# Performance work log

Measured on AMD Instinct MI355X. Metric: run time of the kernel, lower is better.

Reference implementation:

```python
import jax, jax.numpy as jnp
import numpy as np

NUM_CLASSES = 2
TOP_K = 5000
NMS_THRESH = 0.3
CONF_THRESH = 0.05
VAR0, VAR1 = 0.1, 0.2


def setup_inputs() -> dict:
    key = jax.random.key(0)
    k1, k2, k3 = jax.random.split(key, 3)
    B, P = 4, 32768
    loc_data = jax.random.normal(k1, (B, P, 4), dtype=jnp.float32)
    conf_data = jax.random.uniform(k2, (B, P, NUM_CLASSES), dtype=jnp.float32)
    prior_data = jax.random.uniform(k3, (P, 4), dtype=jnp.float32)
    return {"loc_data": loc_data, "conf_data": conf_data, "prior_data": prior_data}


def _detect(loc_data, conf_data, prior_data):
    B = loc_data.shape[0]
    P = prior_data.shape[0]
    loc = loc_data.reshape(B, P, 4)
    conf = conf_data.reshape(B, P, NUM_CLASSES)

    # decode: priors are (cx, cy, w, h); output corner boxes (x1, y1, x2, y2)
    cxcy = prior_data[None, :, :2] + loc[..., :2] * VAR0 * prior_data[None, :, 2:]
    wh = prior_data[None, :, 2:] * jnp.exp(loc[..., 2:] * VAR1)
    boxes = jnp.concatenate([cxcy - 0.5 * wh, cxcy + 0.5 * wh], axis=-1)  # [B,P,4]

    def per_image(bx, sc):  # bx: [P,4], sc: [P] (class-1 scores)
        valid = sc > CONF_THRESH
        masked = jnp.where(valid, sc, -jnp.inf)
        order = jnp.argsort(-masked)[:TOP_K]        # top_k candidates, score-descending
        cb = bx[order]                              # [K,4]
        cs = sc[order]                              # [K]
        cv = valid[order]                           # [K]

        x1, y1, x2, y2 = cb[:, 0], cb[:, 1], cb[:, 2], cb[:, 3]
        area = (x2 - x1) * (y2 - y1)                # [K]
        # pairwise IoU matrix [K,K]
        iw = jnp.maximum(jnp.minimum(x2[:, None], x2[None, :]) - jnp.maximum(x1[:, None], x1[None, :]), 0.0)
        ih = jnp.maximum(jnp.minimum(y2[:, None], y2[None, :]) - jnp.maximum(y1[:, None], y1[None, :]), 0.0)
        inter = iw * ih
        union = area[:, None] + area[None, :] - inter
        suppress = (inter / union) > NMS_THRESH     # suppress if IoU > thresh (keep if <=)

        def step(suppressed, j):
            keep_j = cv[j] & jnp.logical_not(suppressed[j])
            suppressed = suppressed | (keep_j & suppress[j])
            return suppressed, keep_j

        _, kept = jax.lax.scan(step, jnp.zeros((TOP_K,), bool), jnp.arange(TOP_K))

        # pack kept detections (score, x1, y1, x2, y2) to the front, zeros elsewhere
        pos = jnp.where(kept, jnp.cumsum(kept.astype(jnp.int32)) - 1, TOP_K)
        rows = jnp.concatenate([cs[:, None], cb], axis=1)  # [K,5]
        return jnp.zeros((TOP_K, 5), loc_data.dtype).at[pos].set(rows, mode='drop')

    out1 = jax.vmap(per_image)(boxes, conf[..., 1])  # [B,K,5]
    output = jnp.zeros((B, NUM_CLASSES, TOP_K, 5), loc_data.dtype)
    return output.at[:, 1].set(out1)  # class 0 (background) stays zero


def reference(loc_data, conf_data, prior_data):
    return _detect(loc_data, conf_data, prior_data)
```

## Files before the change

### kernel.cpp

```cpp
#include <hip/hip_runtime.h>
#include <hip/hip_bf16.h>
#include <math.h>

#define BB 4
#define PP 32768
#define TOPK 5000
#define NB 4096
#define NBK 20
#define TBPI 210
#define BMW 160
#define TRIW 411872u

#define NV_OFF     0u
#define NC_OFF     64u
#define CS_OFF     256u
#define CB_OFF     80256u
#define HIST_OFF   400256u
#define CNT_OFF    465792u
#define START_OFF  531328u
#define GIDX_OFF   596864u
#define GSC_OFF    1121152u
#define BM_OFF     400256u
#define WS_NEEDED  3742720u

typedef const __attribute__((address_space(1))) unsigned GU1;
struct U4p { unsigned x, y, z, w; };
typedef const __attribute__((address_space(1))) U4p GU4;

__device__ __forceinline__ unsigned toffw(unsigned r) {
    unsigned q = r >> 5, s = r & 31u;
    return r * 160u - 16u * q * (q - 1u) - s * q;
}

__global__ __launch_bounds__(256) void score_hist_kernel(
    const float2* __restrict__ conf, unsigned* __restrict__ hist,
    float2* __restrict__ outz, int outn2)
{
    int i = blockIdx.x * 256 + threadIdx.x;
    if (i < outn2) outz[i] = make_float2(0.0f, 0.0f);
    if (i >= BB * PP) return;
    int b = i >> 15;
    float s = conf[i].y;
    if (s > 0.05f) {
        int bk = (int)(s * 4096.0f);
        bk = bk < 0 ? 0 : (bk > NB - 1 ? NB - 1 : bk);
        atomicAdd(&hist[b * NB + bk], 1u);
    }
}

__global__ __launch_bounds__(256) void scan_hist_kernel(
    const unsigned* __restrict__ hist, unsigned* __restrict__ start,
    int* __restrict__ nvalid, int* __restrict__ ncand)
{
    int b = blockIdx.x;
    int t = threadIdx.x;
    __shared__ unsigned sums[256];
    unsigned local[16];
    unsigned s = 0;
    const unsigned* hb = hist + b * NB;
    #pragma unroll
    for (int k = 0; k < 16; k++) {
        unsigned v = hb[t * 16 + k];
        local[k] = s;
        s += v;
    }
    sums[t] = s;
    __syncthreads();
    for (int off = 1; off < 256; off <<= 1) {
        unsigned v = (t >= off) ? sums[t - off] : 0u;
        __syncthreads();
        sums[t] += v;
        __syncthreads();
    }
    unsigned excl = sums[t] - s;
    unsigned* sb = start + b * NB;
    #pragma unroll
    for (int k = 0; k < 16; k++) sb[t * 16 + k] = excl + local[k];
    if (t == 255) {
        nvalid[b] = (int)sums[255];
        ncand[b] = sums[255] < (unsigned)TOPK ? (int)sums[255] : TOPK;
    }
}

__global__ __launch_bounds__(256) void scatter_group_kernel(
    const float2* __restrict__ conf, const unsigned* __restrict__ start,
    unsigned* __restrict__ cnt, unsigned* __restrict__ gidx,
    float* __restrict__ gscore)
{
    int i = blockIdx.x * 256 + threadIdx.x;
    if (i >= BB * PP) return;
    int b = i >> 15;
    int p = i & (PP - 1);
    float s = conf[i].y;
    if (s > 0.05f) {
        int bk = (int)(s * 4096.0f);
        bk = bk < 0 ? 0 : (bk > NB - 1 ? NB - 1 : bk);
        unsigned o = atomicAdd(&cnt[b * NB + bk], 1u);
        unsigned pos = start[b * NB + bk] + o;
        gidx[b * PP + pos] = (unsigned)p;
        gscore[b * PP + pos] = s;
    }
}

__global__ __launch_bounds__(256) void rank_topk_kernel(
    const unsigned* __restrict__ gidx, const float* __restrict__ gscore,
    const unsigned* __restrict__ start, const unsigned* __restrict__ hist,
    const int* __restrict__ nvalid, const float4* __restrict__ loc,
    const float4* __restrict__ prior,
    float* __restrict__ cs, float4* __restrict__ cb)
{
#pragma clang fp contract(off)
    int i = blockIdx.x * 256 + threadIdx.x;
    if (i >= BB * PP) return;
    int b = i >> 15;
    int pos = i & (PP - 1);
    int nv = nvalid[b];
    if (pos >= nv) return;
    float s = gscore[b * PP + pos];
    unsigned p = gidx[b * PP + pos];
    int bk = (int)(s * 4096.0f);
    bk = bk < 0 ? 0 : (bk > NB - 1 ? NB - 1 : bk);
    unsigned st = start[b * NB + bk];
    unsigned c = hist[b * NB + bk];
    unsigned rank = (unsigned)nv - st - c;
    const float* gs = gscore + b * PP + st;
    const unsigned* gi = gidx + b * PP + st;
    for (unsigned k = 0; k < c; k++) {
        float sk = gs[k];
        unsigned pk = gi[k];
        if (sk > s || (sk == s && pk < p)) rank++;
    }
    if (rank < (unsigned)TOPK) {
        float4 l = loc[b * PP + (int)p];
        float4 pr = prior[p];
        float cx = pr.x + (l.x * 0.1f) * pr.z;
        float cy = pr.y + (l.y * 0.1f) * pr.w;
        float w = pr.z * expf(l.z * 0.2f);
        float h = pr.w * expf(l.w * 0.2f);
        float4 bx;
        bx.x = cx - 0.5f * w;
        bx.y = cy - 0.5f * h;
        bx.z = cx + 0.5f * w;
        bx.w = cy + 0.5f * h;
        cs[b * TOPK + rank] = s;
        cb[(size_t)b * TOPK + rank] = bx;
    }
}

__global__ __launch_bounds__(256) void bitmap_pair_kernel(
    const float4* __restrict__ cb, int img_base, unsigned* __restrict__ bitmap)
{
#pragma clang fp contract(off)
    int p = blockIdx.x / TBPI;
    int t_ = blockIdx.x % TBPI;
    int img = img_base + p;
    unsigned* bmp = bitmap + (size_t)p * TRIW;

    int bi = (int)((sqrtf(8.0f * (float)t_ + 1.0f) - 1.0f) * 0.5f);
    while ((bi + 1) * (bi + 2) / 2 <= t_) bi++;
    while (bi * (bi + 1) / 2 > t_) bi--;
    int bj = t_ - bi * (bi + 1) / 2;

    const float4* cbb = cb + (size_t)img * TOPK;

    __shared__ float4 jb[256];
    __shared__ float ja[256];
    int tid = threadIdx.x;
    int cg = bi * 256 + tid;
    if (cg < TOPK) {
        float4 v = cbb[cg];
        jb[tid] = v;
        ja[tid] = (v.z - v.x) * (v.w - v.y);
    }
    __syncthreads();

    int r = bj * 256 + tid;
    if (r >= TOPK) return;
    float4 bx = cbb[r];
    float areaR = (bx.z - bx.x) * (bx.w - bx.y);
    bool diag = (bi == bj);

    unsigned wds[8];
    #pragma unroll
    for (int w8 = 0; w8 < 8; w8++) {
        unsigned m = 0u;
        int cb0 = w8 * 32;
        for (int k = 0; k < 32; k++) {
            int cl = cb0 + k;
            int c = bi * 256 + cl;
            if (c >= TOPK) break;
            if (diag && c <= r) continue;
            float4 cc = jb[cl];
            float iw = fminf(bx.z, cc.z) - fmaxf(bx.x, cc.x);
            iw = fmaxf(iw, 0.0f);
            float ih = fminf(bx.w, cc.w) - fmaxf(bx.y, cc.y);
            ih = fmaxf(ih, 0.0f);
            float inter = iw * ih;
            float uni = (ja[cl] + areaR) - inter;
            if (inter / uni > 0.3f) m |= (1u << k);
        }
        wds[w8] = m;
    }
    unsigned q = (unsigned)r >> 5;
    unsigned basew = toffw((unsigned)r) - q + 8u * (unsigned)bi;
    int c0 = diag ? (int)(q - 8u * (unsigned)bj) : 0;
    for (int c = c0; c < 8; c++) bmp[basew + (unsigned)c] = wds[c];
}

__global__ __launch_bounds__(576, 1) void solve_scalar_kernel(
    const float* __restrict__ cs, const float4* __restrict__ cb,
    const int* __restrict__ ncand, int img_base,
    const unsigned* __restrict__ bitmap, float* __restrict__ out)
{
    int tid = threadIdx.x;
    int wv = tid >> 6;
    int lane = tid & 63;
    int img = img_base + blockIdx.x;
    int nc = ncand[img];
    const unsigned* bm = bitmap + (size_t)blockIdx.x * TRIW;

    __shared__ __align__(16) unsigned Rl8[8][BMW];
    __shared__ __align__(16) unsigned diab[2][64][4];
    __shared__ unsigned kw[BMW];
    __shared__ unsigned pref[BMW];

    for (int w = tid; w < BMW; w += 576) {
        kw[w] = 0u;
        int lo = w * 32;
        unsigned m;
        if (lo >= nc) m = 0xffffffffu;
        else if (lo + 32 <= nc) m = 0u;
        else m = ~((1u << (nc - lo)) - 1u);
        Rl8[0][w] = m;
    }
    for (int i = tid; i < 7 * BMW; i += 576) Rl8[1 + i / BMW][i % BMW] = 0u;

    int ng = (nc + 63) >> 6;
    unsigned l4 = (unsigned)lane << 2;
    uint4 P0[8], P1[8], P2[8];
    unsigned carry_lo = 0u, carry_hi = 0u;

#define LOADG(BUF, G) do {                                                  \
    int g_ = (G);                                                           \
    if (g_ < ng && lane < 40) {                                             \
        _Pragma("unroll")                                                   \
        for (int rr = 0; rr < 8; rr++) {                                    \
            int j_ = g_ * 64 + (wv - 1) + 8 * rr;                           \
            unsigned jc_ = (unsigned)(j_ < nc ? j_ : nc - 1);               \
            unsigned q_ = jc_ >> 5;                                         \
            GU4* p4_ = (GU4*)(bm + (toffw(jc_) - q_ + l4));                 \
            BUF[rr].x = p4_->x; BUF[rr].y = p4_->y;                         \
            BUF[rr].z = p4_->z; BUF[rr].w = p4_->w;                         \
        }                                                                   \
    }                                                                       \
} while (0)

#define STAGE(SB, G) do {                                                   \
    int g_ = (G);                                                           \
    if (g_ < ng) {                                                          \
        int pa_ = g_ & 1;                                                   \
        if ((g_ & 1) == 0) {                                                \
            int kl_ = g_ >> 1;             \
            if (lane == kl_) {                                              \
                _Pragma("unroll")                                           \
                for (int rr = 0; rr < 8; rr++)                              \
                    *(uint4*)&diab[pa_][(wv - 1) + 8 * rr][0] = SB[rr];     \
            }                                                               \
        } else {                                                            \
            int kl_ = (g_ - 1) >> 1;          \
            if (lane == kl_) {                                              \
                _Pragma("unroll")                                           \
                for (int rr = 0; rr < 8; rr++) {                            \
                    int r_ = (wv - 1) + 8 * rr;                             \
                    diab[pa_][r_][0] = SB[rr].z;                            \
                    diab[pa_][r_][1] = SB[rr].w;                            \
                }                                                           \
            }                                                               \
            if (lane == kl_ + 1) {                                          \
                _Pragma("unroll")                                           \
                for (int rr = 0; rr < 8; rr++) {                            \
                    int r_ = (wv - 1) + 8 * rr;                             \
                    diab[pa_][r_][2] = SB[rr].x;                            \
                    diab[pa_][r_][3] = SB[rr].y;                            \
                }                                                           \
            }                                                               \
        }                                                                   \
    }                                                                       \
} while (0)

#define PHASE(W, FB, SB) do {                                               \
    int w_ = (W);                                                           \
    if (wv == 0) {                                                          \
        int par_ = w_ & 1;                                                  \
        uint2 d01_ = *(const uint2*)&diab[par_][lane][0];                   \
        uint2 d23_ = *(const uint2*)&diab[par_][lane][2];                   \
        unsigned gv_ = 0u;                                                  \
        if (lane < 16) gv_ = Rl8[lane & 7][2 * w_ + (lane >> 3)];           \
        gv_ |= __shfl_xor(gv_, 1);                                          \
        gv_ |= __shfl_xor(gv_, 2);                                          \
        gv_ |= __shfl_xor(gv_, 4);                                          \
        unsigned glo_ = (unsigned)__builtin_amdgcn_readlane((int)gv_, 0);   \
        unsigned ghi_ = (unsigned)__builtin_amdgcn_readlane((int)gv_, 8);   \
        unsigned long long A_ =                                             \
            ~((((unsigned long long)(ghi_ | carry_hi)) << 32)               \
              | (unsigned long long)(glo_ | carry_lo));                     \
        unsigned rlo_ = d01_.x, rhi_ = d01_.y;                              \
        if (lane < 32) rlo_ |= 1u << lane;                                  \
        else           rhi_ |= 1u << (lane & 31);                           \
        unsigned long long K_ = 0ull;                                       \
        while (A_) {                                                        \
            int j_ = __builtin_ctzll(A_);                                   \
            unsigned slo_ = (unsigned)__builtin_amdgcn_readlane((int)rlo_, j_); \
            unsigned shi_ = (unsigned)__builtin_amdgcn_readlane((int)rhi_, j_); \
            K_ |= 1ull << j_;                                               \
            A_ &= ~((((unsigned long long)shi_) << 32)                      \
                    | (unsigned long long)slo_);                            \
        }                                                                   \
        if (lane == 0) {                                                    \
            kw[2 * w_] = (unsigned)K_;                                      \
            kw[2 * w_ + 1] = (unsigned)(K_ >> 32);                          \
        }                                                                   \
        unsigned keep_ = (unsigned)((K_ >> lane) & 1ull);                   \
        unsigned nm_ = 0u - keep_;                                          \
        unsigned nlo_ = d23_.x & nm_, nhi_ = d23_.y & nm_;                  \
        _Pragma("unroll")                                                   \
        for (int mm_ = 32; mm_; mm_ >>= 1) {                                \
            nlo_ |= __shfl_xor(nlo_, mm_);                                  \
            nhi_ |= __shfl_xor(nhi_, mm_);                                  \
        }                                                                   \
        carry_lo = nlo_; carry_hi = nhi_;                                   \
    } else {                                                                \
        if (w_ > 0) {                                                       \
            unsigned klo_ = kw[2 * (w_ - 1)];                               \
            unsigned khi_ = kw[2 * (w_ - 1) + 1];                           \
            unsigned long long Kp_ =                                        \
                (((unsigned long long)khi_) << 32) | klo_;                  \
            uint4 acc_; acc_.x = acc_.y = acc_.z = acc_.w = 0u;             \
            _Pragma("unroll")                                               \
            for (int rr = 0; rr < 8; rr++) {                                \
                int r_ = (wv - 1) + 8 * rr;                                 \
                unsigned a_ = (unsigned)((Kp_ >> r_) & 1ull);               \
                unsigned m_ = 0u - a_;                                      \
                acc_.x |= FB[rr].x & m_; acc_.y |= FB[rr].y & m_;           \
                acc_.z |= FB[rr].z & m_; acc_.w |= FB[rr].w & m_;           \
            }                                                               \
            if (lane < 40) {                                                \
                uint4 cur_ = *(const uint4*)&Rl8[wv - 1][l4];               \
                cur_.x |= acc_.x; cur_.y |= acc_.y;                         \
                cur_.z |= acc_.z; cur_.w |= acc_.w;                         \
                *(uint4*)&Rl8[wv - 1][l4] = cur_;                           \
            }                                                               \
        }                                                                   \
        STAGE(SB, w_ + 1);                                                  \
        LOADG(FB, w_ + 2);                                                  \
    }                                                                       \
    asm volatile("s_waitcnt lgkmcnt(0)" ::: "memory");                      \
    __builtin_amdgcn_s_barrier();                                           \
} while (0)

    if (wv > 0) {
        LOADG(P0, 0);
        LOADG(P1, 1);
    }
    __syncthreads();
    if (wv > 0) STAGE(P0, 0);
    __syncthreads();

    for (int w = 0; w < ng; ) {
        PHASE(w, P2, P1); ++w; if (w >= ng) break;
        PHASE(w, P0, P2); ++w; if (w >= ng) break;
        PHASE(w, P1, P0); ++w;
    }
#undef LOADG
#undef STAGE
#undef PHASE

    __syncthreads();
    if (tid == 0) {
        unsigned s = 0;
        for (int w = 0; w < BMW; w++) { pref[w] = s; s += __popc(kw[w]); }
    }
    __syncthreads();

    const float* csb = cs + img * TOPK;
    const float4* cbb = cb + (size_t)img * TOPK;
    float* outb = out + ((size_t)img * 2 + 1) * TOPK * 5;
    for (int i = tid; i < nc; i += 576) {
        unsigned w = kw[i >> 5];
        if ((w >> (i & 31)) & 1u) {
            unsigned pos = pref[i >> 5] + __popc(w & ((1u << (i & 31)) - 1u));
            float4 bx = cbb[i];
            float* row = outb + (size_t)pos * 5;
            row[0] = csb[i];
            row[1] = bx.x;
            row[2] = bx.y;
            row[3] = bx.z;
            row[4] = bx.w;
        }
    }
}

extern "C" void kernel_launch(void* const* d_in, const int* in_sizes, int n_in,
                              void* d_out, int out_size, void* d_ws, size_t ws_size,
                              hipStream_t stream) {
    if (ws_size < WS_NEEDED) return;

    const float4* loc = (const float4*)d_in[0];
    const float2* conf = (const float2*)d_in[1];
    const float4* prior = (const float4*)d_in[2];
    float* out = (float*)d_out;

    char* ws = (char*)d_ws;
    int* nvalid = (int*)(ws + NV_OFF);
    int* ncand = (int*)(ws + NC_OFF);
    float* cs = (float*)(ws + CS_OFF);
    float4* cb = (float4*)(ws + CB_OFF);
    unsigned* hist = (unsigned*)(ws + HIST_OFF);
    unsigned* cnt = (unsigned*)(ws + CNT_OFF);
    unsigned* start = (unsigned*)(ws + START_OFF);
    unsigned* gidx = (unsigned*)(ws + GIDX_OFF);
    float* gscore = (float*)(ws + GSC_OFF);
    unsigned* bitmap = (unsigned*)(ws + BM_OFF);

    hipError_t e_ = hipMemsetAsync(hist, 0, 2u * BB * NB * sizeof(unsigned),
                                   stream);
    (void)e_;

    int nblk = (BB * PP + 255) / 256;
    score_hist_kernel<<<nblk, 256, 0, stream>>>(conf, hist, (float2*)out,
                                                out_size / 2);
    scan_hist_kernel<<<BB, 256, 0, stream>>>(hist, start, nvalid, ncand);
    scatter_group_kernel<<<nblk, 256, 0, stream>>>(conf, start, cnt, gidx, gscore);
    rank_topk_kernel<<<nblk, 256, 0, stream>>>(gidx, gscore, start, hist, nvalid,
                                               loc, prior, cs, cb);
    for (int g = 0; g < 2; ++g) {
        bitmap_pair_kernel<<<2 * TBPI, 256, 0, stream>>>(cb, 2 * g, bitmap);
        solve_scalar_kernel<<<2, 576, 0, stream>>>(cs, cb, ncand, 2 * g, bitmap, out);
    }
}
```

Before: 345.6 us.

## Run redundant NMS resolve in every wave to drop the one-group-lag carry

Each wave now resolves the 64-candidate diagonal block itself from a shared diagonal tile, so helper waves can OR suppression rows for the current group straight away. Before, they used the previous group's keep mask, and wave 0 carried the next-group suppression through shuffle reductions. This removes the carry shuffles and the one-phase lag, and the staging now keeps only two words per row. In exchange, the serial ctz/readlane loop is repeated in all nine waves and global loads are prefetched three groups ahead, which costs more registers.

```diff
diff --git a/kernel.cpp b/kernel.cpp
--- a/kernel.cpp
+++ b/kernel.cpp
@@ -207,7 +207,7 @@
     for (int c = c0; c < 8; c++) bmp[basew + (unsigned)c] = wds[c];
 }
 
-__global__ __launch_bounds__(576, 1) void solve_scalar_kernel(
+__global__ __launch_bounds__(576, 1) void solve_rd_kernel(
     const float* __restrict__ cs, const float4* __restrict__ cb,
     const int* __restrict__ ncand, int img_base,
     const unsigned* __restrict__ bitmap, float* __restrict__ out)
@@ -220,7 +220,7 @@
     const unsigned* bm = bitmap + (size_t)blockIdx.x * TRIW;
 
     __shared__ __align__(16) unsigned Rl8[8][BMW];
-    __shared__ __align__(16) unsigned diab[2][64][4];
+    __shared__ __align__(8) unsigned diab[2][64][2];
     __shared__ unsigned kw[BMW];
     __shared__ unsigned pref[BMW];
 
@@ -238,7 +238,6 @@
     int ng = (nc + 63) >> 6;
     unsigned l4 = (unsigned)lane << 2;
     uint4 P0[8], P1[8], P2[8];
-    unsigned carry_lo = 0u, carry_hi = 0u;
 
 #define LOADG(BUF, G) do {                                                  \
     int g_ = (G);                                                           \
@@ -257,32 +256,21 @@
 
 #define STAGE(SB, G) do {                                                   \
     int g_ = (G);                                                           \
-    if (g_ < ng) {                                                          \
+    if (g_ < ng && lane == (g_ >> 1)) {                                     \
         int pa_ = g_ & 1;                                                   \
         if ((g_ & 1) == 0) {                                                \
-            int kl_ = g_ >> 1;             \
-            if (lane == kl_) {                                              \
-                _Pragma("unroll")                                           \
-                for (int rr = 0; rr < 8; rr++)                              \
-                    *(uint4*)&diab[pa_][(wv - 1) + 8 * rr][0] = SB[rr];     \
+            _Pragma("unroll")                                               \
+            for (int rr = 0; rr < 8; rr++) {                                \
+                int r_ = (wv - 1) + 8 * rr;                                 \
+                diab[pa_][r_][0] = SB[rr].x;                                \
+                diab[pa_][r_][1] = SB[rr].y;                                \
             }                                                               \
         } else {                                                            \
-            int kl_ = (g_ - 1) >> 1;          \
-            if (lane == kl_) {                                              \
-                _Pragma("unroll")                                           \
-                for (int rr = 0; rr < 8; rr++) {                            \
-                    int r_ = (wv - 1) + 8 * rr;                             \
-                    diab[pa_][r_][0] = SB[rr].z;                            \
-                    diab[pa_][r_][1] = SB[rr].w;                            \
-                }                                                           \
-            }                                                               \
-            if (lane == kl_ + 1) {                                          \
-                _Pragma("unroll")                                           \
-                for (int rr = 0; rr < 8; rr++) {                            \
-                    int r_ = (wv - 1) + 8 * rr;                             \
-                    diab[pa_][r_][2] = SB[rr].x;                            \
-                    diab[pa_][r_][3] = SB[rr].y;                            \
-                }                                                           \
+            _Pragma("unroll")                                               \
+            for (int rr = 0; rr < 8; rr++) {                                \
+                int r_ = (wv - 1) + 8 * rr;                                 \
+                diab[pa_][r_][0] = SB[rr].z;                                \
+                diab[pa_][r_][1] = SB[rr].w;                                \
             }                                                               \
         }                                                                   \
     }                                                                       \
@@ -290,69 +278,54 @@
 
 #define PHASE(W, FB, SB) do {                                               \
     int w_ = (W);                                                           \
+    int par_ = w_ & 1;                                                      \
+                                   \
+    uint2 d01_ = *(const uint2*)&diab[par_][lane][0];                       \
+    unsigned gv_ = 0u;                                                      \
+    if (lane < 16) gv_ = Rl8[lane & 7][2 * w_ + (lane >> 3)];               \
+    gv_ |= __shfl_xor(gv_, 1);                                              \
+    gv_ |= __shfl_xor(gv_, 2);                                              \
+    gv_ |= __shfl_xor(gv_, 4);                                              \
+    unsigned glo_ = (unsigned)__builtin_amdgcn_readlane((int)gv_, 0);       \
+    unsigned ghi_ = (unsigned)__builtin_amdgcn_readlane((int)gv_, 8);       \
+    unsigned long long A_ =                                                 \
+        ~((((unsigned long long)ghi_) << 32) | (unsigned long long)glo_);   \
+    unsigned rlo_ = d01_.x, rhi_ = d01_.y;                                  \
+    if (lane < 32) rlo_ |= 1u << lane;                                      \
+    else           rhi_ |= 1u << (lane & 31);                               \
+    unsigned long long K_ = 0ull;                                           \
+    while (A_) {                                                            \
+        int j_ = __builtin_ctzll(A_);                                       \
+        unsigned slo_ = (unsigned)__builtin_amdgcn_readlane((int)rlo_, j_); \
+        unsigned shi_ = (unsigned)__builtin_amdgcn_readlane((int)rhi_, j_); \
+        K_ |= 1ull << j_;                                                   \
+        A_ &= ~((((unsigned long long)shi_) << 32)                          \
+                | (unsigned long long)slo_);                                \
+    }                                                                       \
     if (wv == 0) {                                                          \
-        int par_ = w_ & 1;                                                  \
-        uint2 d01_ = *(const uint2*)&diab[par_][lane][0];                   \
-        uint2 d23_ = *(const uint2*)&diab[par_][lane][2];                   \
-        unsigned gv_ = 0u;                                                  \
-        if (lane < 16) gv_ = Rl8[lane & 7][2 * w_ + (lane >> 3)];           \
-        gv_ |= __shfl_xor(gv_, 1);                                          \
-        gv_ |= __shfl_xor(gv_, 2);                                          \
-        gv_ |= __shfl_xor(gv_, 4);                                          \
-        unsigned glo_ = (unsigned)__builtin_amdgcn_readlane((int)gv_, 0);   \
-        unsigned ghi_ = (unsigned)__builtin_amdgcn_readlane((int)gv_, 8);   \
-        unsigned long long A_ =                                             \
-            ~((((unsigned long long)(ghi_ | carry_hi)) << 32)               \
-              | (unsigned long long)(glo_ | carry_lo));                     \
-        unsigned rlo_ = d01_.x, rhi_ = d01_.y;                              \
-        if (lane < 32) rlo_ |= 1u << lane;                                  \
-        else           rhi_ |= 1u << (lane & 31);                           \
-        unsigned long long K_ = 0ull;                                       \
-        while (A_) {                                                        \
-            int j_ = __builtin_ctzll(A_);                                   \
-            unsigned slo_ = (unsigned)__builtin_amdgcn_readlane((int)rlo_, j_); \
-            unsigned shi_ = (unsigned)__builtin_amdgcn_readlane((int)rhi_, j_); \
-            K_ |= 1ull << j_;                                               \
-            A_ &= ~((((unsigned long long)shi_) << 32)                      \
-                    | (unsigned long long)slo_);                            \
-        }                                                                   \
         if (lane == 0) {                                                    \
             kw[2 * w_] = (unsigned)K_;                                      \
             kw[2 * w_ + 1] = (unsigned)(K_ >> 32);                          \
         }                                                                   \
-        unsigned keep_ = (unsigned)((K_ >> lane) & 1ull);                   \
-        unsigned nm_ = 0u - keep_;                                          \
-        unsigned nlo_ = d23_.x & nm_, nhi_ = d23_.y & nm_;                  \
+    } else {                                                                \
+                      \
+        uint4 acc_; acc_.x = acc_.y = acc_.z = acc_.w = 0u;                 \
         _Pragma("unroll")                                                   \
-        for (int mm_ = 32; mm_; mm_ >>= 1) {                                \
-            nlo_ |= __shfl_xor(nlo_, mm_);                                  \
-            nhi_ |= __shfl_xor(nhi_, mm_);                                  \
+        for (int rr = 0; rr < 8; rr++) {                                    \
+            int r_ = (wv - 1) + 8 * rr;                                     \
+            unsigned a_ = (unsigned)((K_ >> r_) & 1ull);                    \
+            unsigned m_ = 0u - a_;                                          \
+            acc_.x |= FB[rr].x & m_; acc_.y |= FB[rr].y & m_;               \
+            acc_.z |= FB[rr].z & m_; acc_.w |= FB[rr].w & m_;               \
         }                                                                   \
-        carry_lo = nlo_; carry_hi = nhi_;                                   \
-    } else {                                                                \
-        if (w_ > 0) {                                                       \
-            unsigned klo_ = kw[2 * (w_ - 1)];                               \
-            unsigned khi_ = kw[2 * (w_ - 1) + 1];                           \
-            unsigned long long Kp_ =                                        \
-                (((unsigned long long)khi_) << 32) | klo_;                  \
-            uint4 acc_; acc_.x = acc_.y = acc_.z = acc_.w = 0u;             \
-            _Pragma("unroll")                                               \
-            for (int rr = 0; rr < 8; rr++) {                                \
-                int r_ = (wv - 1) + 8 * rr;                                 \
-                unsigned a_ = (unsigned)((Kp_ >> r_) & 1ull);               \
-                unsigned m_ = 0u - a_;                                      \
-                acc_.x |= FB[rr].x & m_; acc_.y |= FB[rr].y & m_;           \
-                acc_.z |= FB[rr].z & m_; acc_.w |= FB[rr].w & m_;           \
-            }                                                               \
-            if (lane < 40) {                                                \
-                uint4 cur_ = *(const uint4*)&Rl8[wv - 1][l4];               \
-                cur_.x |= acc_.x; cur_.y |= acc_.y;                         \
-                cur_.z |= acc_.z; cur_.w |= acc_.w;                         \
-                *(uint4*)&Rl8[wv - 1][l4] = cur_;                           \
-            }                                                               \
+        if (lane < 40) {                                                    \
+            uint4 cur_ = *(const uint4*)&Rl8[wv - 1][l4];                   \
+            cur_.x |= acc_.x; cur_.y |= acc_.y;                             \
+            cur_.z |= acc_.z; cur_.w |= acc_.w;                             \
+            *(uint4*)&Rl8[wv - 1][l4] = cur_;                               \
         }                                                                   \
         STAGE(SB, w_ + 1);                                                  \
-        LOADG(FB, w_ + 2);                                                  \
+        LOADG(FB, w_ + 3);                                                  \
     }                                                                       \
     asm volatile("s_waitcnt lgkmcnt(0)" ::: "memory");                      \
     __builtin_amdgcn_s_barrier();                                           \
@@ -361,15 +334,16 @@
     if (wv > 0) {
         LOADG(P0, 0);
         LOADG(P1, 1);
+        LOADG(P2, 2);
     }
     __syncthreads();
     if (wv > 0) STAGE(P0, 0);
     __syncthreads();
 
     for (int w = 0; w < ng; ) {
-        PHASE(w, P2, P1); ++w; if (w >= ng) break;
-        PHASE(w, P0, P2); ++w; if (w >= ng) break;
-        PHASE(w, P1, P0); ++w;
+        PHASE(w, P0, P1); ++w; if (w >= ng) break;
+        PHASE(w, P1, P2); ++w; if (w >= ng) break;
+        PHASE(w, P2, P0); ++w;
     }
 #undef LOADG
 #undef STAGE
@@ -435,6 +409,6 @@
                                                loc, prior, cs, cb);
     for (int g = 0; g < 2; ++g) {
         bitmap_pair_kernel<<<2 * TBPI, 256, 0, stream>>>(cb, 2 * g, bitmap);
-        solve_scalar_kernel<<<2, 576, 0, stream>>>(cs, cb, ncand, 2 * g, bitmap, out);
-    }
-}
+        solve_rd_kernel<<<2, 576, 0, stream>>>(cs, cb, ncand, 2 * g, bitmap, out);
+    }
+}
```

Result: slower. 378.2 us (+9.4%).
